# Performance work log

Measured on AMD Instinct MI355X. Metric: run time of the kernel, lower is better.

## Reference

```python
import jax, jax.numpy as jnp
import numpy as np

N, E, F0, H, D, G, C = 10000, 150000, 128, 8, 64, 64, 10
HD = H * D
SLOPE = 0.01  # LeakyReLU negative slope (alpha)
EPS = 1e-5    # BatchNorm eps


def gat_layer(x, src, dst, W, a_src, a_dst, b):
    # x: [N, Fin] -> out: [N, H*D]; standard multi-head GAT with concat
    n = x.shape[0]
    h = (x @ W).reshape(n, H, D)                       # [N,H,D]
    e_src = jnp.einsum('nhd,hd->nh', h, a_src)         # [N,H]
    e_dst = jnp.einsum('nhd,hd->nh', h, a_dst)
    e = e_src[src] + e_dst[dst]                        # [E,H]
    e = jnp.where(e > 0, e, SLOPE * e)                 # LeakyReLU
    m = jax.ops.segment_max(e, dst, num_segments=n)    # per-dst max for stable softmax
    ex = jnp.exp(e - m[dst])
    denom = jax.ops.segment_sum(ex, dst, num_segments=n)
    att = ex / denom[dst]                              # [E,H]
    msg = h[src] * att[:, :, None]                     # [E,H,D]
    out = jax.ops.segment_sum(msg, dst, num_segments=n).reshape(n, HD)
    return jax.nn.elu(out + b)


def hgnn_forward(x, edge_index, batch,
                 W0, as0, ad0, b0, W1, as1, ad1, b1,
                 W2, as2, ad2, b2, W3, as3, ad3, b3,
                 mW1, mb1, gamma, beta, mW2, mb2):
    src, dst = edge_index[0], edge_index[1]
    x0 = gat_layer(x, src, dst, W0, as0, ad0, b0)      # init_graph
    x1 = gat_layer(x0, src, dst, W1, as1, ad1, b1)     # head
    x2 = gat_layer(x1, src, dst, W2, as2, ad2, b2)     # body
    x3 = x0 + x2                                       # residual
    xt = gat_layer(x3, src, dst, W3, as3, ad3, b3)     # tail
    xc = jnp.concatenate((xt, x1, x2, x3), axis=1)     # [N, 4*HD]
    pooled = jax.ops.segment_max(xc, batch, num_segments=G)
    pooled = jnp.where(jnp.isfinite(pooled), pooled, 0.0)
    # MLP: Linear -> BatchNorm1d (batch-stats) -> ReLU -> Linear
    z = pooled @ mW1 + mb1
    mu = jnp.mean(z, axis=0)
    var = jnp.mean((z - mu) ** 2, axis=0)
    z = (z - mu) / jnp.sqrt(var + EPS) * gamma + beta
    z = jax.nn.relu(z)
    return z @ mW2 + mb2                               # [G, C]


def setup_inputs() -> dict:
    key = jax.random.key(0)
    ks = jax.random.split(key, 12)
    x = jax.random.normal(ks[0], (N, F0), jnp.float32)
    edge_index = jax.random.randint(ks[1], (2, E), 0, N, dtype=jnp.int32)
    batch = jnp.sort(jax.random.randint(ks[2], (N,), 0, G, dtype=jnp.int32))

    def layer_params(k, fin):
        k1, k2, k3 = jax.random.split(k, 3)
        return (0.1 * jax.random.normal(k1, (fin, HD), jnp.float32),
                0.1 * jax.random.normal(k2, (H, D), jnp.float32),
                0.1 * jax.random.normal(k3, (H, D), jnp.float32),
                jnp.zeros((HD,), jnp.float32))

    W0, as0, ad0, b0 = layer_params(ks[3], F0)
    W1, as1, ad1, b1 = layer_params(ks[4], HD)
    W2, as2, ad2, b2 = layer_params(ks[5], HD)
    W3, as3, ad3, b3 = layer_params(ks[6], HD)
    mW1 = 0.05 * jax.random.normal(ks[7], (4 * HD, HD), jnp.float32)
    mb1 = jnp.zeros((HD,), jnp.float32)
    gamma = jnp.ones((HD,), jnp.float32)
    beta = jnp.zeros((HD,), jnp.float32)
    mW2 = 0.05 * jax.random.normal(ks[8], (HD, C), jnp.float32)
    mb2 = jnp.zeros((C,), jnp.float32)
    return dict(x=x, edge_index=edge_index, batch=batch,
                W0=W0, as0=as0, ad0=ad0, b0=b0,
                W1=W1, as1=as1, ad1=ad1, b1=b1,
                W2=W2, as2=as2, ad2=ad2, b2=b2,
                W3=W3, as3=as3, ad3=ad3, b3=b3,
                mW1=mW1, mb1=mb1, gamma=gamma, beta=beta, mW2=mW2, mb2=mb2)


def reference(x, edge_index, batch,
              W0, as0, ad0, b0, W1, as1, ad1, b1,
              W2, as2, ad2, b2, W3, as3, ad3, b3,
              mW1, mb1, gamma, beta, mW2, mb2):
    return hgnn_forward(x, edge_index, batch,
                        W0, as0, ad0, b0, W1, as1, ad1, b1,
                        W2, as2, ad2, b2, W3, as3, ad3, b3,
                        mW1, mb1, gamma, beta, mW2, mb2)
```

## Files before the change

### kernel.cpp

```cpp
#include <hip/hip_runtime.h>

typedef unsigned short u16;
typedef __bf16 bfv8 __attribute__((ext_vector_type(8)));
typedef float f32x16 __attribute__((ext_vector_type(16)));

#define HDIM 512
#define NHEAD 8
#define GNUM 64
#define CNUM 10
#define SLOPE 0.01f
#define BNEPS 1e-5f
#define PSPLIT 8

__device__ __forceinline__ float b2f(u16 u) { return __uint_as_float(((unsigned)u) << 16); }
__device__ __forceinline__ u16 f2b(float f) {
    unsigned u = __float_as_uint(f);
    u += 0x7FFFu + ((u >> 16) & 1u);
    return (u16)(u >> 16);
}
__device__ __forceinline__ void splitbf(float v, u16& hi, u16& lo) {
    u16 h = f2b(v);
    hi = h;
    lo = f2b(v - b2f(h));
}

__global__ void sentinel_kernel(float* out, int n, float val) {
    int i = blockIdx.x * 256 + threadIdx.x;
    if (i < n) out[i] = val;
}

__global__ void zero_i32_kernel(int* __restrict__ p, int n) {
    int i = blockIdx.x * 256 + threadIdx.x;
    if (i < n) p[i] = 0;
}

__device__ __forceinline__ void wsplit_body(const float* __restrict__ W, u16* __restrict__ Whi,
                                            u16* __restrict__ Wlo, int K) {
    __shared__ float tile[64][65];
    int kb = blockIdx.x * 64, nb = blockIdx.y * 64;
    int t = threadIdx.x;
    #pragma unroll
    for (int i = 0; i < 16; i++) {
        int idx = t + i * 256;
        int r = idx >> 6, c = idx & 63;
        tile[r][c] = W[(size_t)(kb + r) * HDIM + nb + c];
    }
    __syncthreads();
    #pragma unroll
    for (int i = 0; i < 16; i++) {
        int idx = t + i * 256;
        int r = idx >> 6, c = idx & 63;
        float v = tile[c][r];
        u16 hi, lo;
        splitbf(v, hi, lo);
        size_t o = (size_t)(nb + r) * K + kb + c;
        Whi[o] = hi;
        Wlo[o] = lo;
    }
}

__global__ void wsplit_kernel(const float* __restrict__ W, u16* __restrict__ Whi,
                              u16* __restrict__ Wlo, int K) {
    wsplit_body(W, Whi, Wlo, K);
}

__global__ void wsplit3_kernel(const float* __restrict__ W1, const float* __restrict__ W2,
                               const float* __restrict__ W3,
                               u16* __restrict__ h1, u16* __restrict__ l1,
                               u16* __restrict__ h2, u16* __restrict__ l2,
                               u16* __restrict__ h3, u16* __restrict__ l3) {
    const float* W = (blockIdx.z == 0) ? W1 : (blockIdx.z == 1) ? W2 : W3;
    u16* Wh = (blockIdx.z == 0) ? h1 : (blockIdx.z == 1) ? h2 : h3;
    u16* Wl = (blockIdx.z == 0) ? l1 : (blockIdx.z == 1) ? l2 : l3;
    wsplit_body(W, Wh, Wl, HDIM);
}

__global__ void xsplit_kernel(const float* __restrict__ x, u16* __restrict__ hi,
                              u16* __restrict__ lo, int n) {
    int i = blockIdx.x * 256 + threadIdx.x;
    if (i < n) splitbf(x[i], hi[i], lo[i]);
}

__global__ __launch_bounds__(256, 2) void gemm_split(const u16* __restrict__ Ah,
                                                     const u16* __restrict__ Al,
                                                     const u16* __restrict__ Bh,
                                                     const u16* __restrict__ Bl,
                                                     const float* __restrict__ a_src,
                                                     const float* __restrict__ a_dst,
                                                     u16* __restrict__ Chi,
                                                     float* __restrict__ es,
                                                     float* __restrict__ ed, int M, int K) {
    __shared__ u16 sAh[128 * 40];
    __shared__ u16 sAl[128 * 40];
    __shared__ u16 sBh[64 * 40];
    __shared__ u16 sBl[64 * 40];
    __shared__ float sE[128][2][2];
    int t = threadIdx.x;
    int id = blockIdx.x;
    int nrt = gridDim.x >> 3;
    int w = (id & 7) * nrt + (id >> 3);
    int rt = w >> 3, ct = w & 7;
    int bm = rt * 128, bn = ct * 64;
    int hh = ct;
    int wv = t >> 6, lane = t & 63;
    int wm = (wv >> 1) * 64, wn = (wv & 1) * 32;
    int l32 = lane & 31, kh = lane >> 5;

    int ar0 = (2 * t) >> 2, ac0 = ((2 * t) & 3) * 8;
    int ar1 = (2 * t + 1) >> 2, ac1 = ((2 * t + 1) & 3) * 8;
    int br = t >> 2, bc = (t & 3) * 8;

    f32x16 acc[2];
    for (int m = 0; m < 2; m++)
        for (int r = 0; r < 16; r++) acc[m][r] = 0.f;

    bool ok0 = (bm + ar0) < M, ok1 = (bm + ar1) < M;
    const u16* Ahp0 = Ah + (size_t)(bm + ar0) * K + ac0;
    const u16* Alp0 = Al + (size_t)(bm + ar0) * K + ac0;
    const u16* Ahp1 = Ah + (size_t)(bm + ar1) * K + ac1;
    const u16* Alp1 = Al + (size_t)(bm + ar1) * K + ac1;
    const u16* Bhp = Bh + (size_t)(bn + br) * K + bc;
    const u16* Blp = Bl + (size_t)(bn + br) * K + bc;

    for (int kt = 0; kt < K; kt += 32) {
        int4 a0h = make_int4(0, 0, 0, 0), a0l = a0h, a1h = a0h, a1l = a0h;
        if (ok0) { a0h = *(const int4*)(Ahp0 + kt); a0l = *(const int4*)(Alp0 + kt); }
        if (ok1) { a1h = *(const int4*)(Ahp1 + kt); a1l = *(const int4*)(Alp1 + kt); }
        int4 bvh = *(const int4*)(Bhp + kt);
        int4 bvl = *(const int4*)(Blp + kt);
        __syncthreads();
        *(int4*)&sAh[ar0 * 40 + ac0] = a0h;
        *(int4*)&sAl[ar0 * 40 + ac0] = a0l;
        *(int4*)&sAh[ar1 * 40 + ac1] = a1h;
        *(int4*)&sAl[ar1 * 40 + ac1] = a1l;
        *(int4*)&sBh[br * 40 + bc] = bvh;
        *(int4*)&sBl[br * 40 + bc] = bvl;
        __syncthreads();
        #pragma unroll
        for (int ks = 0; ks < 32; ks += 16) {
            int ko = ks + kh * 8;
            bfv8 a0 = *(bfv8*)&sAh[(wm + l32) * 40 + ko];
            bfv8 a0lo = *(bfv8*)&sAl[(wm + l32) * 40 + ko];
            bfv8 a1 = *(bfv8*)&sAh[(wm + 32 + l32) * 40 + ko];
            bfv8 a1lo = *(bfv8*)&sAl[(wm + 32 + l32) * 40 + ko];
            bfv8 b = *(bfv8*)&sBh[(wn + l32) * 40 + ko];
            bfv8 blo = *(bfv8*)&sBl[(wn + l32) * 40 + ko];
            acc[0] = __builtin_amdgcn_mfma_f32_32x32x16_bf16(a0lo, b, acc[0], 0, 0, 0);
            acc[0] = __builtin_amdgcn_mfma_f32_32x32x16_bf16(a0, blo, acc[0], 0, 0, 0);
            acc[0] = __builtin_amdgcn_mfma_f32_32x32x16_bf16(a0, b, acc[0], 0, 0, 0);
            acc[1] = __builtin_amdgcn_mfma_f32_32x32x16_bf16(a1lo, b, acc[1], 0, 0, 0);
            acc[1] = __builtin_amdgcn_mfma_f32_32x32x16_bf16(a1, blo, acc[1], 0, 0, 0);
            acc[1] = __builtin_amdgcn_mfma_f32_32x32x16_bf16(a1, b, acc[1], 0, 0, 0);
        }
    }
    float asv = a_src[hh * 64 + wn + l32];
    float adv = a_dst[hh * 64 + wn + l32];
    int col = bn + wn + l32;
    #pragma unroll
    for (int mt = 0; mt < 2; mt++)
        #pragma unroll
        for (int r = 0; r < 16; r++) {
            float v = acc[mt][r];
            int lr = wm + mt * 32 + (r & 3) + 8 * (r >> 2) + 4 * kh;
            int row = bm + lr;
            if (row < M) Chi[(size_t)row * HDIM + col] = f2b(v);
            float s1 = v * asv, s2 = v * adv;
            #pragma unroll
            for (int msk = 1; msk <= 16; msk <<= 1) {
                s1 += __shfl_xor(s1, msk);
                s2 += __shfl_xor(s2, msk);
            }
            if (l32 == 0) { sE[lr][wv & 1][0] = s1; sE[lr][wv & 1][1] = s2; }
        }
    __syncthreads();
    if (t < 128) {
        int row = bm + t;
        if (row < M) {
            es[row * NHEAD + hh] = sE[t][0][0] + sE[t][1][0];
            ed[row * NHEAD + hh] = sE[t][0][1] + sE[t][1][1];
        }
    }
}

__global__ void hist_kernel(const int* __restrict__ ei, int* __restrict__ deg, int E) {
    int e = blockIdx.x * 256 + threadIdx.x;
    if (e < E) atomicAdd(&deg[ei[E + e]], 1);
}

__global__ void scan_kernel(const int* __restrict__ deg, int* __restrict__ offs,
                            int* __restrict__ cursor, int n) {
    __shared__ int lds[1024];
    int t = threadIdx.x;
    const int CH = 16;
    int base = t * CH;
    int local[CH];
    int s = 0;
    for (int i = 0; i < CH; i++) {
        int idx = base + i;
        local[i] = (idx < n) ? deg[idx] : 0;
        s += local[i];
    }
    lds[t] = s;
    __syncthreads();
    for (int off = 1; off < 1024; off <<= 1) {
        int v = lds[t];
        int add = (t >= off) ? lds[t - off] : 0;
        __syncthreads();
        lds[t] = v + add;
        __syncthreads();
    }
    int ex = (t == 0) ? 0 : lds[t - 1];
    for (int i = 0; i < CH; i++) {
        int idx = base + i;
        if (idx < n) { offs[idx] = ex; cursor[idx] = ex; ex += local[i]; }
    }
}

__global__ void scatter_kernel(const int* __restrict__ ei, int* __restrict__ cursor,
                               int* __restrict__ ssrc, int E) {
    int e = blockIdx.x * 256 + threadIdx.x;
    if (e < E) {
        int p = atomicAdd(&cursor[ei[E + e]], 1);
        ssrc[p] = ei[e];
    }
}

__global__ void agg_kernel(const u16* __restrict__ hh_buf, const float* __restrict__ es,
                           const float* __restrict__ ed, const int* __restrict__ offs,
                           const int* __restrict__ deg, const int* __restrict__ ssrc,
                           const float* __restrict__ bias,
                           u16* __restrict__ ohi, u16* __restrict__ olo,
                           const u16* __restrict__ rhi, const u16* __restrict__ rlo,
                           u16* __restrict__ qhi, u16* __restrict__ qlo, int n) {
    int node = blockIdx.x * 4 + (threadIdx.x >> 6);
    int lane = threadIdx.x & 63;
    if (node >= n) return;
    int hh = lane >> 3, f = lane * 8;
    float edv = ed[node * NHEAD + hh];
    int st = offs[node], cnt = deg[node];

    float m = -INFINITY, den = 0.f;
    float acc[8] = {0.f, 0.f, 0.f, 0.f, 0.f, 0.f, 0.f, 0.f};
    int i = 0;
    for (; i + 2 <= cnt; i += 2) {
        int s0 = ssrc[st + i];
        int s1 = ssrc[st + i + 1];
        float e0 = es[s0 * NHEAD + hh] + edv;
        float e1 = es[s1 * NHEAD + hh] + edv;
        union { int4 v; u16 u[8]; } U0, U1;
        U0.v = *(const int4*)(hh_buf + (size_t)s0 * HDIM + f);
        U1.v = *(const int4*)(hh_buf + (size_t)s1 * HDIM + f);
        e0 = e0 > 0.f ? e0 : SLOPE * e0;
        e1 = e1 > 0.f ? e1 : SLOPE * e1;
        float mn = fmaxf(m, fmaxf(e0, e1));
        float sc = __expf(m - mn);
        float w0 = __expf(e0 - mn);
        float w1 = __expf(e1 - mn);
        den = den * sc + w0 + w1;
        #pragma unroll
        for (int j = 0; j < 8; j++)
            acc[j] = acc[j] * sc + w0 * b2f(U0.u[j]) + w1 * b2f(U1.u[j]);
        m = mn;
    }
    if (i < cnt) {
        int s0 = ssrc[st + i];
        float e0 = es[s0 * NHEAD + hh] + edv;
        union { int4 v; u16 u[8]; } U0;
        U0.v = *(const int4*)(hh_buf + (size_t)s0 * HDIM + f);
        e0 = e0 > 0.f ? e0 : SLOPE * e0;
        float mn = fmaxf(m, e0);
        float sc = __expf(m - mn);
        float w0 = __expf(e0 - mn);
        den = den * sc + w0;
        #pragma unroll
        for (int j = 0; j < 8; j++) acc[j] = acc[j] * sc + w0 * b2f(U0.u[j]);
    }
    float inv = den > 0.f ? 1.f / den : 0.f;
    union { int4 v; u16 u[8]; } Hi, Lo;
    float o[8];
    #pragma unroll
    for (int j = 0; j < 8; j++) {
        float v = acc[j] * inv + bias[f + j];
        o[j] = v > 0.f ? v : __expf(v) - 1.f;
        splitbf(o[j], Hi.u[j], Lo.u[j]);
    }
    size_t base = (size_t)node * HDIM + f;
    *(int4*)&ohi[base] = Hi.v;
    *(int4*)&olo[base] = Lo.v;
    if (rhi) {
        union { int4 v; u16 u[8]; } Rh, Rl, Qh, Ql;
        Rh.v = *(const int4*)&rhi[base];
        Rl.v = *(const int4*)&rlo[base];
        #pragma unroll
        for (int j = 0; j < 8; j++) {
            float v = o[j] + b2f(Rh.u[j]) + b2f(Rl.u[j]);
            splitbf(v, Qh.u[j], Ql.u[j]);
        }
        *(int4*)&qhi[base] = Qh.v;
        *(int4*)&qlo[base] = Ql.v;
    }
}

__global__ void pool1_kernel(const u16* __restrict__ s0h, const u16* __restrict__ s1h,
                             const u16* __restrict__ s2h, const u16* __restrict__ s3h,
                             const int* __restrict__ batch, float* __restrict__ partial, int n) {
    int g = blockIdx.x, b = blockIdx.y, c = blockIdx.z;
    int t = threadIdx.x;
    const u16* hs[4] = {s0h, s1h, s2h, s3h};
    const u16* sh = hs[b];
    int lo = 0, hi = n;
    while (lo < hi) { int mid = (lo + hi) >> 1; if (batch[mid] < g) lo = mid + 1; else hi = mid; }
    int start = lo;
    lo = start; hi = n;
    while (lo < hi) { int mid = (lo + hi) >> 1; if (batch[mid] < g + 1) lo = mid + 1; else hi = mid; }
    int end = lo;
    int len = end - start;
    int cb = start + (int)(((long long)len * c) / PSPLIT);
    int ce = start + (int)(((long long)len * (c + 1)) / PSPLIT);
    float mx0 = -INFINITY, mx1 = -INFINITY;
    for (int i = cb; i < ce; i++) {
        size_t ro = (size_t)i * HDIM;
        mx0 = fmaxf(mx0, b2f(sh[ro + t]));
        mx1 = fmaxf(mx1, b2f(sh[ro + 256 + t]));
    }
    size_t pb = (size_t)((g * 4 + b) * PSPLIT + c) * 512;
    partial[pb + t] = mx0;
    partial[pb + 256 + t] = mx1;
}

__global__ void pool2_kernel(const float* __restrict__ partial, float* __restrict__ pooled) {
    int g = blockIdx.x, b = blockIdx.y;
    int t = threadIdx.x;
    float mx0 = -INFINITY, mx1 = -INFINITY;
    for (int c = 0; c < PSPLIT; c++) {
        size_t pb = (size_t)((g * 4 + b) * PSPLIT + c) * 512;
        mx0 = fmaxf(mx0, partial[pb + t]);
        mx1 = fmaxf(mx1, partial[pb + 256 + t]);
    }
    if (!isfinite(mx0)) mx0 = 0.f;
    if (!isfinite(mx1)) mx1 = 0.f;
    pooled[g * 2048 + b * 512 + t] = mx0;
    pooled[g * 2048 + b * 512 + 256 + t] = mx1;
}

__global__ void zinit_kernel(float* __restrict__ z, const float* __restrict__ mb1) {
    int i = blockIdx.x * 256 + threadIdx.x;
    if (i < GNUM * HDIM) z[i] = mb1[i & (HDIM - 1)];
}

__global__ __launch_bounds__(256) void mlp1_splitk(const float* __restrict__ pooled,
                                                   const float* __restrict__ mW1,
                                                   float* __restrict__ z) {
    __shared__ float sp[256];
    int g = blockIdx.x, kc = blockIdx.y * 256;
    int t = threadIdx.x;
    sp[t] = pooled[g * 2048 + kc + t];
    __syncthreads();
    float acc0 = 0.f, acc1 = 0.f;
    const float* wp = mW1 + (size_t)kc * HDIM;
    #pragma unroll 8
    for (int k = 0; k < 256; k++) {
        float pv = sp[k];
        acc0 += pv * wp[(size_t)k * HDIM + t];
        acc1 += pv * wp[(size_t)k * HDIM + 256 + t];
    }
    atomicAdd(&z[g * HDIM + t], acc0);
    atomicAdd(&z[g * HDIM + 256 + t], acc1);
}

__global__ void bn_relu_kernel(const float* __restrict__ z, const float* __restrict__ gammaf,
                               const float* __restrict__ betaf, float* __restrict__ zn) {
    int col = blockIdx.x;
    int g = threadIdx.x;
    float v = z[g * HDIM + col];
    float s = v;
    for (int o = 32; o > 0; o >>= 1) s += __shfl_xor(s, o);
    float mu = s * (1.f / 64.f);
    float d = v - mu;
    float s2 = d * d;
    for (int o = 32; o > 0; o >>= 1) s2 += __shfl_xor(s2, o);
    float var = s2 * (1.f / 64.f);
    float o = d * rsqrtf(var + BNEPS) * gammaf[col] + betaf[col];
    zn[g * HDIM + col] = fmaxf(o, 0.f);
}

__global__ void final_kernel(const float* __restrict__ zn, const float* __restrict__ mW2,
                             const float* __restrict__ mb2, float* __restrict__ out) {
    int t = threadIdx.x;
    if (t >= GNUM * CNUM) return;
    int g = t / CNUM, c = t - g * CNUM;
    float acc = mb2[c];
    for (int k = 0; k < HDIM; k++) acc += zn[g * HDIM + k] * mW2[k * CNUM + c];
    out[t] = acc;
}

extern "C" void kernel_launch(void* const* d_in, const int* in_sizes, int n_in,
                              void* d_out, int out_size, void* d_ws, size_t ws_size,
                              hipStream_t stream) {
    const float* x = (const float*)d_in[0];
    const int* ei = (const int*)d_in[1];
    const int* batch = (const int*)d_in[2];
    const float* Wm[4] = {(const float*)d_in[3], (const float*)d_in[7],
                          (const float*)d_in[11], (const float*)d_in[15]};
    const float* Asc[4] = {(const float*)d_in[4], (const float*)d_in[8],
                           (const float*)d_in[12], (const float*)d_in[16]};
    const float* Adc[4] = {(const float*)d_in[5], (const float*)d_in[9],
                           (const float*)d_in[13], (const float*)d_in[17]};
    const float* Bb[4] = {(const float*)d_in[6], (const float*)d_in[10],
                          (const float*)d_in[14], (const float*)d_in[18]};
    const float* mW1 = (const float*)d_in[19];
    const float* mb1 = (const float*)d_in[20];
    const float* gammaf = (const float*)d_in[21];
    const float* betaf = (const float*)d_in[22];
    const float* mW2 = (const float*)d_in[23];
    const float* mb2 = (const float*)d_in[24];
    (void)n_in;

    int N = in_sizes[2];
    int E = in_sizes[1] / 2;
    int F0 = in_sizes[0] / N;

    char* p = (char*)d_ws;
    auto alloc = [&](size_t bytes) -> char* {
        char* r = p;
        p += (bytes + 255) & ~(size_t)255;
        return r;
    };
    u16 *Wh[4], *Wl[4];
    Wh[0] = (u16*)alloc((size_t)HDIM * F0 * 2);
    Wl[0] = (u16*)alloc((size_t)HDIM * F0 * 2);
    for (int l = 1; l < 4; l++) {
        Wh[l] = (u16*)alloc((size_t)HDIM * HDIM * 2);
        Wl[l] = (u16*)alloc((size_t)HDIM * HDIM * 2);
    }
    u16* xinh = (u16*)alloc((size_t)N * F0 * 2);
    u16* xinl = (u16*)alloc((size_t)N * F0 * 2);
    u16* hhi = (u16*)alloc((size_t)N * HDIM * 2);
    u16 *xh[4], *xl[4];
    for (int l = 0; l < 4; l++) {
        xh[l] = (u16*)alloc((size_t)N * HDIM * 2);
        xl[l] = (u16*)alloc((size_t)N * HDIM * 2);
    }
    float* es = (float*)alloc((size_t)N * NHEAD * 4);
    float* ed = (float*)alloc((size_t)N * NHEAD * 4);
    int* deg = (int*)alloc((size_t)N * 4);
    int* offs = (int*)alloc((size_t)N * 4);
    int* cursor = (int*)alloc((size_t)N * 4);
    int* ssrc = (int*)alloc((size_t)E * 4);
    float* partial = (float*)alloc((size_t)GNUM * 4 * PSPLIT * 512 * 4);
    float* pooled = (float*)alloc((size_t)GNUM * 4 * HDIM * 4);
    float* z = (float*)alloc((size_t)GNUM * HDIM * 4);
    float* zn = (float*)alloc((size_t)GNUM * HDIM * 4);

    if ((size_t)(p - (char*)d_ws) > ws_size) {
        sentinel_kernel<<<(out_size + 255) / 256, 256, 0, stream>>>((float*)d_out, out_size, 999.f);
        return;
    }

    {
        dim3 wg0(F0 / 64, HDIM / 64);
        wsplit_kernel<<<wg0, 256, 0, stream>>>(Wm[0], Wh[0], Wl[0], F0);
        dim3 wg3(HDIM / 64, HDIM / 64, 3);
        wsplit3_kernel<<<wg3, 256, 0, stream>>>(Wm[1], Wm[2], Wm[3],
                                                Wh[1], Wl[1], Wh[2], Wl[2], Wh[3], Wl[3]);
    }
    xsplit_kernel<<<(N * F0 + 255) / 256, 256, 0, stream>>>(x, xinh, xinl, N * F0);

    zero_i32_kernel<<<(N + 255) / 256, 256, 0, stream>>>(deg, N);
    hist_kernel<<<(E + 255) / 256, 256, 0, stream>>>(ei, deg, E);
    scan_kernel<<<1, 1024, 0, stream>>>(deg, offs, cursor, N);
    scatter_kernel<<<(E + 255) / 256, 256, 0, stream>>>(ei, cursor, ssrc, E);

    const u16* linh[4] = {xinh, xh[0], xh[1], xh[3]};
    const u16* linl[4] = {xinl, xl[0], xl[1], xl[3]};
    int lK[4] = {F0, HDIM, HDIM, HDIM};
    u16* louth[4] = {xh[0], xh[1], xh[2], xh[0]};
    u16* loutl[4] = {xl[0], xl[1], xl[2], xl[0]};
    int nrt = (N + 127) / 128;
    int gemm_blocks = nrt * 8;
    int agg_blocks = (N + 3) / 4;
    for (int L = 0; L < 4; L++) {
        gemm_split<<<gemm_blocks, 256, 0, stream>>>(linh[L], linl[L], Wh[L], Wl[L],
                                                    Asc[L], Adc[L], hhi, es, ed, N, lK[L]);
        const u16* rh = (L == 2) ? xh[0] : nullptr;
        const u16* rl = (L == 2) ? xl[0] : nullptr;
        u16* qh = (L == 2) ? xh[3] : nullptr;
        u16* ql = (L == 2) ? xl[3] : nullptr;
        agg_kernel<<<agg_blocks, 256, 0, stream>>>(hhi, es, ed, offs, deg, ssrc, Bb[L],
                                                   louth[L], loutl[L], rh, rl, qh, ql, N);
    }

    dim3 pool1_grid(GNUM, 4, PSPLIT);
    pool1_kernel<<<pool1_grid, 256, 0, stream>>>(xh[0], xh[1], xh[2], xh[3],
                                                 batch, partial, N);
    dim3 pool2_grid(GNUM, 4);
    pool2_kernel<<<pool2_grid, 256, 0, stream>>>(partial, pooled);

    zinit_kernel<<<(GNUM * HDIM + 255) / 256, 256, 0, stream>>>(z, mb1);
    dim3 mlp_grid(GNUM, 8);
    mlp1_splitk<<<mlp_grid, 256, 0, stream>>>(pooled, mW1, z);
    bn_relu_kernel<<<HDIM, 64, 0, stream>>>(z, gammaf, betaf, zn);
    final_kernel<<<1, 640, 0, stream>>>(zn, mW2, mb2, (float*)d_out);
}
```

Baseline: 475.7 us.

## Prefetch GEMM tiles into registers, fuse z init into pool2, parallelize final matvec

The GEMM now loads the next K-tile from global memory into registers while the current tile's MFMAs run, and its launch bound is raised to 3 blocks per CU. The separate zinit kernel is folded into pool2, removing one launch. The final classifier matvec moves from a single 640-thread block with serial 512-long loops to a 64x10 grid that does a wave-level reduction. The prefetch and higher occupancy target both add register pressure, which could cause spills in the GEMM.

```diff
diff --git a/kernel.cpp b/kernel.cpp
--- a/kernel.cpp
+++ b/kernel.cpp
@@ -81,7 +81,7 @@
     if (i < n) splitbf(x[i], hi[i], lo[i]);
 }
 
-__global__ __launch_bounds__(256, 2) void gemm_split(const u16* __restrict__ Ah,
+__global__ __launch_bounds__(256, 3) void gemm_split(const u16* __restrict__ Ah,
                                                      const u16* __restrict__ Al,
                                                      const u16* __restrict__ Bh,
                                                      const u16* __restrict__ Bl,
@@ -122,12 +122,13 @@
     const u16* Bhp = Bh + (size_t)(bn + br) * K + bc;
     const u16* Blp = Bl + (size_t)(bn + br) * K + bc;
 
+    int4 a0h = make_int4(0, 0, 0, 0), a0l = a0h, a1h = a0h, a1l = a0h;
+    if (ok0) { a0h = *(const int4*)(Ahp0); a0l = *(const int4*)(Alp0); }
+    if (ok1) { a1h = *(const int4*)(Ahp1); a1l = *(const int4*)(Alp1); }
+    int4 bvh = *(const int4*)(Bhp);
+    int4 bvl = *(const int4*)(Blp);
+
     for (int kt = 0; kt < K; kt += 32) {
-        int4 a0h = make_int4(0, 0, 0, 0), a0l = a0h, a1h = a0h, a1l = a0h;
-        if (ok0) { a0h = *(const int4*)(Ahp0 + kt); a0l = *(const int4*)(Alp0 + kt); }
-        if (ok1) { a1h = *(const int4*)(Ahp1 + kt); a1l = *(const int4*)(Alp1 + kt); }
-        int4 bvh = *(const int4*)(Bhp + kt);
-        int4 bvl = *(const int4*)(Blp + kt);
         __syncthreads();
         *(int4*)&sAh[ar0 * 40 + ac0] = a0h;
         *(int4*)&sAl[ar0 * 40 + ac0] = a0l;
@@ -136,6 +137,14 @@
         *(int4*)&sBh[br * 40 + bc] = bvh;
         *(int4*)&sBl[br * 40 + bc] = bvl;
         __syncthreads();
+        int ktn = kt + 32;
+        if (ktn < K) {
+            a0h = make_int4(0, 0, 0, 0); a0l = a0h; a1h = a0h; a1l = a0h;
+            if (ok0) { a0h = *(const int4*)(Ahp0 + ktn); a0l = *(const int4*)(Alp0 + ktn); }
+            if (ok1) { a1h = *(const int4*)(Ahp1 + ktn); a1l = *(const int4*)(Alp1 + ktn); }
+            bvh = *(const int4*)(Bhp + ktn);
+            bvl = *(const int4*)(Blp + ktn);
+        }
         #pragma unroll
         for (int ks = 0; ks < 32; ks += 16) {
             int ko = ks + kh * 8;
@@ -328,7 +337,8 @@
     partial[pb + 256 + t] = mx1;
 }
 
-__global__ void pool2_kernel(const float* __restrict__ partial, float* __restrict__ pooled) {
+__global__ void pool2_kernel(const float* __restrict__ partial, float* __restrict__ pooled,
+                             const float* __restrict__ mb1, float* __restrict__ z) {
     int g = blockIdx.x, b = blockIdx.y;
     int t = threadIdx.x;
     float mx0 = -INFINITY, mx1 = -INFINITY;
@@ -341,11 +351,10 @@
     if (!isfinite(mx1)) mx1 = 0.f;
     pooled[g * 2048 + b * 512 + t] = mx0;
     pooled[g * 2048 + b * 512 + 256 + t] = mx1;
-}
-
-__global__ void zinit_kernel(float* __restrict__ z, const float* __restrict__ mb1) {
-    int i = blockIdx.x * 256 + threadIdx.x;
-    if (i < GNUM * HDIM) z[i] = mb1[i & (HDIM - 1)];
+    if (t < 128) {
+        int col = b * 128 + t;
+        z[g * HDIM + col] = mb1[col];
+    }
 }
 
 __global__ __launch_bounds__(256) void mlp1_splitk(const float* __restrict__ pooled,
@@ -386,12 +395,13 @@
 
 __global__ void final_kernel(const float* __restrict__ zn, const float* __restrict__ mW2,
                              const float* __restrict__ mb2, float* __restrict__ out) {
-    int t = threadIdx.x;
-    if (t >= GNUM * CNUM) return;
-    int g = t / CNUM, c = t - g * CNUM;
-    float acc = mb2[c];
-    for (int k = 0; k < HDIM; k++) acc += zn[g * HDIM + k] * mW2[k * CNUM + c];
-    out[t] = acc;
+    int g = blockIdx.x, c = blockIdx.y;
+    int lane = threadIdx.x;
+    float acc = 0.f;
+    #pragma unroll
+    for (int k = lane; k < HDIM; k += 64) acc += zn[g * HDIM + k] * mW2[k * CNUM + c];
+    for (int o = 32; o > 0; o >>= 1) acc += __shfl_down(acc, o);
+    if (lane == 0) out[g * CNUM + c] = acc + mb2[c];
 }
 
 extern "C" void kernel_launch(void* const* d_in, const int* in_sizes, int n_in,
@@ -494,11 +504,11 @@
     pool1_kernel<<<pool1_grid, 256, 0, stream>>>(xh[0], xh[1], xh[2], xh[3],
                                                  batch, partial, N);
     dim3 pool2_grid(GNUM, 4);
-    pool2_kernel<<<pool2_grid, 256, 0, stream>>>(partial, pooled);
-
-    zinit_kernel<<<(GNUM * HDIM + 255) / 256, 256, 0, stream>>>(z, mb1);
+    pool2_kernel<<<pool2_grid, 256, 0, stream>>>(partial, pooled, mb1, z);
+
     dim3 mlp_grid(GNUM, 8);
     mlp1_splitk<<<mlp_grid, 256, 0, stream>>>(pooled, mW1, z);
     bn_relu_kernel<<<HDIM, 64, 0, stream>>>(z, gammaf, betaf, zn);
-    final_kernel<<<1, 640, 0, stream>>>(zn, mW2, mb2, (float*)d_out);
-}
+    dim3 final_grid(GNUM, CNUM);
+    final_kernel<<<final_grid, 64, 0, stream>>>(zn, mW2, mb2, (float*)d_out);
+}
```

Measured after the change: 436.3 us. 1.09x faster.
